# Kernel optimization log

Measured on AMD Instinct MI355X. Metric: run time of the kernel, lower is better.

Reference implementation:

```python
import jax, jax.numpy as jnp
import numpy as np
from jax import lax

B, N, R, L = 16, 256, 24, 32
MEAN_STOP_TIME_S = 60.0
AVG_TRANSFER_WAIT_TIME_S = 300.0
SYMMETRIC_ROUTES = True
INF = jnp.inf


def setup_inputs() -> dict:
    key = jax.random.key(0)
    k1, k2, k3 = jax.random.split(key, 3)
    drive_times = jax.random.uniform(k1, (B, N, N), jnp.float32) * 1000.0 + 30.0
    demand = jax.random.uniform(k2, (B, N, N), jnp.float32) * 10.0
    demand = demand * (1.0 - jnp.eye(N, dtype=jnp.float32))  # no self-demand
    batch_routes = jax.random.randint(k3, (B, R, L), 0, N, dtype=jnp.int32)
    return {"drive_times": drive_times, "demand": demand, "batch_routes": batch_routes}


def _route_edges_and_legs(routes, dtm):
    # routes: [B,R,L] node ids (no -1 padding in this setup); dtm: [B,N,N]
    b = jnp.arange(B)[:, None, None]
    sf, st = routes[:, :, :-1], routes[:, :, 1:]
    leg_fwd = dtm[b, sf, st] + MEAN_STOP_TIME_S            # [B,R,L-1]
    zero = jnp.zeros((B, R, 1), dtm.dtype)
    cum_f = jnp.concatenate([zero, jnp.cumsum(leg_fwd, -1)], -1)  # [B,R,L]
    tri = jnp.triu(jnp.ones((L, L), dtype=bool), 1)
    # ride time from stop position i to position j>i along the route
    t_f = jnp.where(tri, cum_f[:, :, None, :] - cum_f[:, :, :, None], INF)
    b4 = jnp.arange(B)[:, None, None, None]
    src = jnp.broadcast_to(routes[:, :, :, None], (B, R, L, L))
    dst = jnp.broadcast_to(routes[:, :, None, :], (B, R, L, L))
    edge = jnp.full((B, N, N), INF, dtm.dtype)
    edge = edge.at[b4, src, dst].min(t_f)
    leg_rev = None
    if SYMMETRIC_ROUTES:
        leg_rev = dtm[b, st, sf] + MEAN_STOP_TIME_S        # reverse-direction legs
        cum_r = jnp.concatenate([zero, jnp.cumsum(leg_rev, -1)], -1)
        t_r = jnp.where(tri, cum_r[:, :, None, :] - cum_r[:, :, :, None], INF)
        edge = edge.at[b4, dst, src].min(t_r)              # ride from s_j back to s_i
    return edge, leg_fwd, leg_rev


def _floyd_warshall(edge):
    # batched FW, also tracking hop count of shortest paths
    idx = jnp.arange(N)
    dist = edge.at[:, idx, idx].set(0.0)
    offdiag = ~jnp.eye(N, dtype=bool)
    hops = jnp.where(jnp.isfinite(dist) & offdiag, 1.0, 0.0)

    def body(carry, k):
        d, h = carry
        dc = lax.dynamic_slice_in_dim(d, k, 1, axis=2)  # [B,N,1]
        dr = lax.dynamic_slice_in_dim(d, k, 1, axis=1)  # [B,1,N]
        hc = lax.dynamic_slice_in_dim(h, k, 1, axis=2)
        hr = lax.dynamic_slice_in_dim(h, k, 1, axis=1)
        alt = dc + dr
        better = alt < d
        return (jnp.where(better, alt, d), jnp.where(better, hc + hr, h)), None

    (dist, hops), _ = lax.scan(body, (dist, hops), idx)
    return dist, hops


def reference(drive_times, demand, batch_routes):
    edge, leg_fwd, leg_rev = _route_edges_and_legs(batch_routes, drive_times)
    dist, hops = _floyd_warshall(edge)
    nopath = jnp.isinf(dist)
    path_lens = jnp.where(nopath, 0.0, hops + 1.0)  # n nodes on path (diag -> 1)
    transfers = jnp.where(path_lens == 0.0, 0.0, path_lens - 2.0)
    trip_times = jnp.where(nopath, 0.0, dist + transfers * AVG_TRANSFER_WAIT_TIME_S)
    total_demand_time = (demand * trip_times).sum((1, 2))
    total_transfers = (demand * transfers).sum((1, 2))
    unserved_demand = jnp.where(nopath, demand, 0.0).sum((1, 2))
    total_demand = demand.sum((1, 2))
    n_disconnected = (nopath & (demand > 0)).sum((1, 2))
    buckets = [jnp.where(transfers == float(ii), demand, 0.0).sum((1, 2)) for ii in range(3)]
    d_un = jnp.where(transfers > 2.0, demand, 0.0).sum((1, 2)) + unserved_demand
    trips_at_transfers = jnp.stack(buckets + [d_un], axis=1)  # [B,4]
    total_route_time = leg_fwd.sum((1, 2))
    if SYMMETRIC_ROUTES:
        total_route_time = total_route_time + leg_rev.sum((1, 2))
    return (total_demand_time, total_route_time, trips_at_transfers,
            total_demand, unserved_demand, total_transfers, trip_times,
            n_disconnected)
```

## Files before the change

kernel.cpp:

```cpp
#include <hip/hip_runtime.h>

#define BB 16
#define NL 256
#define RR 24
#define LL 32
#define NN (NL*NL)
#define BNN (BB*NN)
#define TT 64

#define O_TDT 0
#define O_RT  16
#define O_TAT 32
#define O_TD  96
#define O_UNS 112
#define O_TTR 128
#define O_TT  144
#define O_ND  1048720

#define HSC 9.3132257461547852e-10
#define H2  1073741824.0
#define HMASK 8191

#define RIDX(r, c2) (((r)<<6) + ((((c2) ^ ((r)&31)))<<1))
#define LDD(A, r, c2) (*(double2*)&A[RIDX((r),(c2))])

__global__ __launch_bounds__(1024) void k_init(double2* __restrict__ dist2, float* __restrict__ acc){
    int idx = blockIdx.x*1024 + threadIdx.x;
    double inf = __builtin_huge_val();
    double2 v = make_double2(inf, inf);
    int q = (idx*2) & (NN-1);
    int r = q % 257;
    if (r == 0)   v.x = 0.0;
    if (r == 256) v.y = 0.0;
    dist2[idx] = v;
    if (blockIdx.x == 0 && threadIdx.x < 256) acc[threadIdx.x] = 0.f;
}

__global__ void k_routes(const float* __restrict__ dtm, const int* __restrict__ routes,
                         unsigned long long* __restrict__ dist, float* __restrict__ acc){
    int br = blockIdx.x; int b = br / RR, r = br % RR;
    int lane = threadIdx.x;
    __shared__ int   s[LL];
    __shared__ float lf[LL], lr[LL], cf[LL], cr[LL];
    if (lane < LL) s[lane] = routes[(b*RR + r)*LL + lane];
    __syncthreads();
    if (lane < LL-1){
        int a0 = s[lane], a1 = s[lane+1];
        const float* dt = dtm + b*NN;
        lf[lane] = dt[a0*NL + a1] + 60.0f;
        lr[lane] = dt[a1*NL + a0] + 60.0f;
    }
    __syncthreads();
    if (lane == 0){
        float af = 0.f, ar = 0.f;
        cf[0] = 0.f; cr[0] = 0.f;
        for (int l = 0; l < LL-1; l++){
            af += lf[l]; ar += lr[l];
            cf[l+1] = af; cr[l+1] = ar;
        }
        atomicAdd(&acc[b*16 + 1], af + ar);
    }
    __syncthreads();
    for (int p = lane; p < LL*LL; p += 64){
        int i = p >> 5, j = p & 31;
        if (j > i){
            double vf = (double)(cf[j] - cf[i]) + HSC;
            double vr = (double)(cr[j] - cr[i]) + HSC;
            atomicMin(&dist[b*NN + s[i]*NL + s[j]], (unsigned long long)__double_as_longlong(vf));
            atomicMin(&dist[b*NN + s[j]*NL + s[i]], (unsigned long long)__double_as_longlong(vr));
        }
    }
}

__global__ __launch_bounds__(512) void k_fw_round(
        const double* __restrict__ src, double* __restrict__ dst, int kb){
    int b  = blockIdx.y;
    int m  = blockIdx.x;
    int ti = m >> 2, tj = m & 3;
    int t  = threadIdx.x;
    int rp  = (t >> 4) * 2;
    int cch = t & 15;
    int c04 = cch * 4;
    __shared__ double KD[4096];
    __shared__ double BD[4096];
    const double* Kg = src + b*NN + kb*TT*(NL+1);
    const double* Bg = src + b*NN + kb*TT*NL + tj*TT;
    const double* Cg = src + b*NN + ti*TT*NL + kb*TT;
    const double* Dg = src + b*NN + ti*TT*NL + tj*TT;

    double c0[2][4], d0[2][4];
    #pragma unroll
    for (int i = 0; i < 2; i++){
        double2 ca = *(const double2*)(Cg + (rp+i)*NL + c04);
        double2 cb = *(const double2*)(Cg + (rp+i)*NL + c04 + 2);
        c0[i][0]=ca.x; c0[i][1]=ca.y; c0[i][2]=cb.x; c0[i][3]=cb.y;
        double2 da = *(const double2*)(Dg + (rp+i)*NL + c04);
        double2 db = *(const double2*)(Dg + (rp+i)*NL + c04 + 2);
        d0[i][0]=da.x; d0[i][1]=da.y; d0[i][2]=db.x; d0[i][3]=db.y;
    }

    #pragma unroll
    for (int u = 0; u < 2; u++){
        int fid = u*512 + t;
        int row = fid >> 4, cc = fid & 15;
        const double* kp = Kg + row*NL + cc*4;
        double2 k0 = *(const double2*)kp, k1 = *(const double2*)(kp+2);
        const double* bp = Bg + row*NL + cc*4;
        double2 b0 = *(const double2*)bp, b1 = *(const double2*)(bp+2);
        LDD(KD,row,cc*2)   = k0; LDD(KD,row,cc*2+1) = k1;
        LDD(BD,row,cc*2)   = b0; LDD(BD,row,cc*2+1) = b1;
    }
    __syncthreads();

    for (int skb = 0; skb < 4; skb++){
        int s0 = skb*16, sc2 = skb*8;
        if (t < 64){
            int i = t >> 2, jg = t & 3, rr = s0 + i, cb = sc2 + jg*2;
            double2 m0 = LDD(KD, rr, cb), m1 = LDD(KD, rr, cb+1);
            double md[4] = {m0.x, m0.y, m1.x, m1.y};
            #pragma unroll
            for (int k = 0; k < 16; k++){
                double rd[4];
                #pragma unroll
                for (int c = 0; c < 4; c++) rd[c] = __shfl(md[c], (k<<2)|jg);
                double cd = __shfl(md[k&3], (i<<2)|(k>>2));
                #pragma unroll
                for (int c = 0; c < 4; c++) md[c] = fmin(md[c], cd + rd[c]);
            }
            LDD(KD, rr, cb)   = make_double2(md[0], md[1]);
            LDD(KD, rr, cb+1) = make_double2(md[2], md[3]);
        }
        __syncthreads();
        double sd[4];
        int wrow, wc2;
        if (t < 256){
            int rsr = s0 + (t >> 4);
            wrow = rsr; wc2 = (t & 15)*2;
            double2 v0 = LDD(KD, rsr, wc2), v1 = LDD(KD, rsr, wc2+1);
            sd[0]=v0.x; sd[1]=v0.y; sd[2]=v1.x; sd[3]=v1.y;
            #pragma unroll
            for (int k = 0; k < 16; k++){
                double ad = KD[RIDX(rsr, sc2+(k>>1)) + (k&1)];
                double2 b0 = LDD(KD, s0+k, wc2), b1 = LDD(KD, s0+k, wc2+1);
                sd[0] = fmin(sd[0], ad + b0.x);
                sd[1] = fmin(sd[1], ad + b0.y);
                sd[2] = fmin(sd[2], ad + b1.x);
                sd[3] = fmin(sd[3], ad + b1.y);
            }
        } else {
            int t2 = t - 256;
            int csr = t2 >> 2;
            wrow = csr; wc2 = sc2 + (t2 & 3)*2;
            double2 v0 = LDD(KD, csr, wc2), v1 = LDD(KD, csr, wc2+1);
            sd[0]=v0.x; sd[1]=v0.y; sd[2]=v1.x; sd[3]=v1.y;
            #pragma unroll
            for (int k = 0; k < 16; k++){
                double ad = KD[RIDX(csr, sc2+(k>>1)) + (k&1)];
                double2 b0 = LDD(KD, s0+k, wc2), b1 = LDD(KD, s0+k, wc2+1);
                sd[0] = fmin(sd[0], ad + b0.x);
                sd[1] = fmin(sd[1], ad + b0.y);
                sd[2] = fmin(sd[2], ad + b1.x);
                sd[3] = fmin(sd[3], ad + b1.y);
            }
        }
        __syncthreads();
        LDD(KD, wrow, wc2)   = make_double2(sd[0], sd[1]);
        LDD(KD, wrow, wc2+1) = make_double2(sd[2], sd[3]);
        __syncthreads();
        double dd[2][4];
        #pragma unroll
        for (int i = 0; i < 2; i++){
            double2 v0 = LDD(KD, rp+i, cch*2), v1 = LDD(KD, rp+i, cch*2+1);
            dd[i][0]=v0.x; dd[i][1]=v0.y; dd[i][2]=v1.x; dd[i][3]=v1.y;
        }
        #pragma unroll
        for (int q4 = 0; q4 < 4; q4++){
            double a[2][4], bm[4][4];
            #pragma unroll
            for (int i = 0; i < 2; i++){
                double2 a0 = LDD(KD, rp+i, sc2+q4*2), a1 = LDD(KD, rp+i, sc2+q4*2+1);
                a[i][0]=a0.x; a[i][1]=a0.y; a[i][2]=a1.x; a[i][3]=a1.y;
            }
            int kr = s0 + q4*4;
            #pragma unroll
            for (int q = 0; q < 4; q++){
                double2 b0 = LDD(KD, kr+q, cch*2), b1 = LDD(KD, kr+q, cch*2+1);
                bm[q][0]=b0.x; bm[q][1]=b0.y; bm[q][2]=b1.x; bm[q][3]=b1.y;
            }
            #pragma unroll
            for (int q = 0; q < 4; q++)
            #pragma unroll
            for (int i = 0; i < 2; i++)
            #pragma unroll
            for (int j = 0; j < 4; j++)
                dd[i][j] = fmin(dd[i][j], a[i][q] + bm[q][j]);
        }
        __syncthreads();
        #pragma unroll
        for (int i = 0; i < 2; i++){
            LDD(KD, rp+i, cch*2)   = make_double2(dd[i][0], dd[i][1]);
            LDD(KD, rp+i, cch*2+1) = make_double2(dd[i][2], dd[i][3]);
        }
        __syncthreads();
    }

    double inf = __builtin_huge_val();
    double md[2][4];
    #pragma unroll
    for (int i = 0; i < 2; i++)
    #pragma unroll
    for (int j = 0; j < 4; j++) md[i][j] = inf;
    #pragma unroll 4
    for (int q4 = 0; q4 < 16; q4++){
        double a[2][4], bm[4][4];
        #pragma unroll
        for (int i = 0; i < 2; i++){
            double2 a0 = LDD(KD, rp+i, q4*2), a1 = LDD(KD, rp+i, q4*2+1);
            a[i][0]=a0.x; a[i][1]=a0.y; a[i][2]=a1.x; a[i][3]=a1.y;
        }
        int kr = q4*4;
        #pragma unroll
        for (int q = 0; q < 4; q++){
            double2 b0 = LDD(BD, kr+q, cch*2), b1 = LDD(BD, kr+q, cch*2+1);
            bm[q][0]=b0.x; bm[q][1]=b0.y; bm[q][2]=b1.x; bm[q][3]=b1.y;
        }
        #pragma unroll
        for (int q = 0; q < 4; q++)
        #pragma unroll
        for (int i = 0; i < 2; i++)
        #pragma unroll
        for (int j = 0; j < 4; j++)
            md[i][j] = fmin(md[i][j], a[i][q] + bm[q][j]);
    }
    __syncthreads();
    #pragma unroll
    for (int i = 0; i < 2; i++){
        LDD(BD, rp+i, cch*2)   = make_double2(md[i][0], md[i][1]);
        LDD(BD, rp+i, cch*2+1) = make_double2(md[i][2], md[i][3]);
        LDD(KD, rp+i, cch*2)   = make_double2(c0[i][0], c0[i][1]);
        LDD(KD, rp+i, cch*2+1) = make_double2(c0[i][2], c0[i][3]);
    }
    __syncthreads();

    double dd[2][4];
    #pragma unroll
    for (int i = 0; i < 2; i++)
    #pragma unroll
    for (int j = 0; j < 4; j++) dd[i][j] = d0[i][j];
    #pragma unroll 4
    for (int q4 = 0; q4 < 16; q4++){
        double a[2][4], bm[4][4];
        #pragma unroll
        for (int i = 0; i < 2; i++){
            double2 a0 = LDD(KD, rp+i, q4*2), a1 = LDD(KD, rp+i, q4*2+1);
            a[i][0]=a0.x; a[i][1]=a0.y; a[i][2]=a1.x; a[i][3]=a1.y;
        }
        int kr = q4*4;
        #pragma unroll
        for (int q = 0; q < 4; q++){
            double2 b0 = LDD(BD, kr+q, cch*2), b1 = LDD(BD, kr+q, cch*2+1);
            bm[q][0]=b0.x; bm[q][1]=b0.y; bm[q][2]=b1.x; bm[q][3]=b1.y;
        }
        #pragma unroll
        for (int q = 0; q < 4; q++)
        #pragma unroll
        for (int i = 0; i < 2; i++)
        #pragma unroll
        for (int j = 0; j < 4; j++)
            dd[i][j] = fmin(dd[i][j], a[i][q] + bm[q][j]);
    }
    double* Od = dst + b*NN + ti*TT*NL + tj*TT;
    #pragma unroll
    for (int i = 0; i < 2; i++){
        *(double2*)(Od + (rp+i)*NL + c04)     = make_double2(dd[i][0], dd[i][1]);
        *(double2*)(Od + (rp+i)*NL + c04 + 2) = make_double2(dd[i][2], dd[i][3]);
    }
}

__global__ __launch_bounds__(1024) void k_epi(const double2* __restrict__ dist2,
        const float4* __restrict__ demand4, float* __restrict__ out, float* __restrict__ acc){
    int b = blockIdx.y;
    int fid = (b*NN >> 2) + blockIdx.x*1024 + threadIdx.x;
    long long q2 = (long long)fid * 2;
    double2 va = dist2[q2], vb = dist2[q2+1];
    double vs[4] = {va.x, va.y, vb.x, vb.y};
    float4 mv = demand4[fid];
    float ms[4] = {mv.x, mv.y, mv.z, mv.w};
    float s0=0,s1=0,s2=0,s3=0,s4=0,s5=0,s6=0,s7=0,s8=0;
    float tts[4];
    #pragma unroll
    for (int e = 0; e < 4; e++){
        double v = vs[e];
        bool np = !(v < 1e37);
        double vv = np ? 0.0 : v;
        int h = (int)(((long long)(vv * H2)) & (long long)HMASK);
        float d = (float)vv;
        float dm = ms[e];
        float pl = np ? 0.f : (float)(h + 1);
        float tr = (pl == 0.f) ? 0.f : pl - 2.f;
        float tt = np ? 0.f : d + tr*300.f;
        tts[e] = tt;
        s0 += dm*tt;
        s1 += dm*tr;
        s2 += np ? dm : 0.f;
        s3 += dm;
        s4 += (np && dm > 0.f) ? 1.f : 0.f;
        s5 += (tr == 0.f) ? dm : 0.f;
        s6 += (tr == 1.f) ? dm : 0.f;
        s7 += (tr == 2.f) ? dm : 0.f;
        s8 += (tr > 2.f) ? dm : 0.f;
    }
    ((float4*)(out + O_TT))[fid] = make_float4(tts[0],tts[1],tts[2],tts[3]);
    #define RED(x) { x += __shfl_down(x,32); x += __shfl_down(x,16); x += __shfl_down(x,8); \
                     x += __shfl_down(x,4);  x += __shfl_down(x,2);  x += __shfl_down(x,1); }
    RED(s0) RED(s1) RED(s2) RED(s3) RED(s4) RED(s5) RED(s6) RED(s7) RED(s8)
    __shared__ float red[16][9];
    int w = threadIdx.x >> 6;
    if ((threadIdx.x & 63) == 0){
        red[w][0]=s0; red[w][1]=s1; red[w][2]=s2; red[w][3]=s3; red[w][4]=s4;
        red[w][5]=s5; red[w][6]=s6; red[w][7]=s7; red[w][8]=s8;
    }
    __syncthreads();
    if (threadIdx.x < 9){
        float v = 0.f;
        #pragma unroll
        for (int ww = 0; ww < 16; ww++) v += red[ww][threadIdx.x];
        int slot = (threadIdx.x == 0) ? 0 : threadIdx.x + 1;
        atomicAdd(&acc[b*16 + slot], v);
    }
    __syncthreads();
    __shared__ int isLast;
    if (threadIdx.x == 0){
        unsigned prev = atomicAdd((unsigned int*)(acc + 255), 1u);
        isLast = (prev == 255u) ? 1 : 0;
    }
    __syncthreads();
    if (isLast && threadIdx.x < BB){
        int bb = threadIdx.x;
        float a[10];
        #pragma unroll
        for (int s = 0; s < 10; s++) a[s] = atomicAdd(&acc[bb*16 + s], 0.f);
        out[O_TDT + bb] = a[0];
        out[O_RT  + bb] = a[1];
        out[O_TAT + 4*bb + 0] = a[6];
        out[O_TAT + 4*bb + 1] = a[7];
        out[O_TAT + 4*bb + 2] = a[8];
        out[O_TAT + 4*bb + 3] = a[9] + a[3];
        out[O_TD  + bb] = a[4];
        out[O_UNS + bb] = a[3];
        out[O_TTR + bb] = a[2];
        out[O_ND  + bb] = a[5];
    }
}

extern "C" void kernel_launch(void* const* d_in, const int* in_sizes, int n_in,
                              void* d_out, int out_size, void* d_ws, size_t ws_size,
                              hipStream_t stream){
    (void)in_sizes; (void)n_in; (void)out_size; (void)ws_size;
    const float* dtm    = (const float*)d_in[0];
    const float* demand = (const float*)d_in[1];
    const int*   routes = (const int*)d_in[2];
    float* out   = (float*)d_out;
    double* distA = (double*)d_ws;
    double* distB = distA + BNN;
    float*  acc   = (float*)(distB + BNN);

    k_init  <<<512, 1024, 0, stream>>>((double2*)distA, acc);
    k_routes<<<BB*RR,  64, 0, stream>>>(dtm, routes, (unsigned long long*)distA, acc);
    k_fw_round<<<dim3(16,BB), 512, 0, stream>>>(distA, distB, 0);
    k_fw_round<<<dim3(16,BB), 512, 0, stream>>>(distB, distA, 1);
    k_fw_round<<<dim3(16,BB), 512, 0, stream>>>(distA, distB, 2);
    k_fw_round<<<dim3(16,BB), 512, 0, stream>>>(distB, distA, 3);
    k_epi<<<dim3(16,BB), 1024, 0, stream>>>((const double2*)distA,
                                            (const float4*)demand, out, acc);
}
```

Baseline: 238.4 us.

## Double FW-round block size to 1024 threads with 2x2 per-thread tiles

```diff
diff --git a/kernel.cpp b/kernel.cpp
--- a/kernel.cpp
+++ b/kernel.cpp
@@ -23,6 +23,7 @@
 
 #define RIDX(r, c2) (((r)<<6) + ((((c2) ^ ((r)&31)))<<1))
 #define LDD(A, r, c2) (*(double2*)&A[RIDX((r),(c2))])
+#define ELEM(A, r, c) A[RIDX((r), (c)>>1) + ((c)&1)]
 
 __global__ __launch_bounds__(1024) void k_init(double2* __restrict__ dist2, float* __restrict__ acc){
     int idx = blockIdx.x*1024 + threadIdx.x;
@@ -72,15 +73,14 @@
     }
 }
 
-__global__ __launch_bounds__(512) void k_fw_round(
+__global__ __launch_bounds__(1024, 4) void k_fw_round(
         const double* __restrict__ src, double* __restrict__ dst, int kb){
     int b  = blockIdx.y;
     int m  = blockIdx.x;
     int ti = m >> 2, tj = m & 3;
     int t  = threadIdx.x;
-    int rp  = (t >> 4) * 2;
-    int cch = t & 15;
-    int c04 = cch * 4;
+    int r0 = (t >> 5) << 1;
+    int c2 = t & 31;
     __shared__ double KD[4096];
     __shared__ double BD[4096];
     const double* Kg = src + b*NN + kb*TT*(NL+1);
@@ -88,27 +88,19 @@
     const double* Cg = src + b*NN + ti*TT*NL + kb*TT;
     const double* Dg = src + b*NN + ti*TT*NL + tj*TT;
 
-    double c0[2][4], d0[2][4];
+    double2 c0[2], d0[2];
     #pragma unroll
     for (int i = 0; i < 2; i++){
-        double2 ca = *(const double2*)(Cg + (rp+i)*NL + c04);
-        double2 cb = *(const double2*)(Cg + (rp+i)*NL + c04 + 2);
-        c0[i][0]=ca.x; c0[i][1]=ca.y; c0[i][2]=cb.x; c0[i][3]=cb.y;
-        double2 da = *(const double2*)(Dg + (rp+i)*NL + c04);
-        double2 db = *(const double2*)(Dg + (rp+i)*NL + c04 + 2);
-        d0[i][0]=da.x; d0[i][1]=da.y; d0[i][2]=db.x; d0[i][3]=db.y;
+        c0[i] = *(const double2*)(Cg + (r0+i)*NL + c2*2);
+        d0[i] = *(const double2*)(Dg + (r0+i)*NL + c2*2);
     }
 
     #pragma unroll
     for (int u = 0; u < 2; u++){
-        int fid = u*512 + t;
-        int row = fid >> 4, cc = fid & 15;
-        const double* kp = Kg + row*NL + cc*4;
-        double2 k0 = *(const double2*)kp, k1 = *(const double2*)(kp+2);
-        const double* bp = Bg + row*NL + cc*4;
-        double2 b0 = *(const double2*)bp, b1 = *(const double2*)(bp+2);
-        LDD(KD,row,cc*2)   = k0; LDD(KD,row,cc*2+1) = k1;
-        LDD(BD,row,cc*2)   = b0; LDD(BD,row,cc*2+1) = b1;
+        int fid = u*1024 + t;
+        int row = fid >> 5, cc = fid & 31;
+        LDD(KD, row, cc) = *(const double2*)(Kg + row*NL + cc*2);
+        LDD(BD, row, cc) = *(const double2*)(Bg + row*NL + cc*2);
     }
     __syncthreads();
 
@@ -117,164 +109,118 @@
         if (t < 64){
             int i = t >> 2, jg = t & 3, rr = s0 + i, cb = sc2 + jg*2;
             double2 m0 = LDD(KD, rr, cb), m1 = LDD(KD, rr, cb+1);
-            double md[4] = {m0.x, m0.y, m1.x, m1.y};
+            double md4[4] = {m0.x, m0.y, m1.x, m1.y};
             #pragma unroll
             for (int k = 0; k < 16; k++){
                 double rd[4];
                 #pragma unroll
-                for (int c = 0; c < 4; c++) rd[c] = __shfl(md[c], (k<<2)|jg);
-                double cd = __shfl(md[k&3], (i<<2)|(k>>2));
+                for (int c = 0; c < 4; c++) rd[c] = __shfl(md4[c], (k<<2)|jg);
+                double cd = __shfl(md4[k&3], (i<<2)|(k>>2));
                 #pragma unroll
-                for (int c = 0; c < 4; c++) md[c] = fmin(md[c], cd + rd[c]);
+                for (int c = 0; c < 4; c++) md4[c] = fmin(md4[c], cd + rd[c]);
             }
-            LDD(KD, rr, cb)   = make_double2(md[0], md[1]);
-            LDD(KD, rr, cb+1) = make_double2(md[2], md[3]);
-        }
-        __syncthreads();
-        double sd[4];
-        int wrow, wc2;
-        if (t < 256){
-            int rsr = s0 + (t >> 4);
-            wrow = rsr; wc2 = (t & 15)*2;
-            double2 v0 = LDD(KD, rsr, wc2), v1 = LDD(KD, rsr, wc2+1);
-            sd[0]=v0.x; sd[1]=v0.y; sd[2]=v1.x; sd[3]=v1.y;
-            #pragma unroll
-            for (int k = 0; k < 16; k++){
-                double ad = KD[RIDX(rsr, sc2+(k>>1)) + (k&1)];
-                double2 b0 = LDD(KD, s0+k, wc2), b1 = LDD(KD, s0+k, wc2+1);
-                sd[0] = fmin(sd[0], ad + b0.x);
-                sd[1] = fmin(sd[1], ad + b0.y);
-                sd[2] = fmin(sd[2], ad + b1.x);
-                sd[3] = fmin(sd[3], ad + b1.y);
-            }
-        } else {
-            int t2 = t - 256;
-            int csr = t2 >> 2;
-            wrow = csr; wc2 = sc2 + (t2 & 3)*2;
-            double2 v0 = LDD(KD, csr, wc2), v1 = LDD(KD, csr, wc2+1);
-            sd[0]=v0.x; sd[1]=v0.y; sd[2]=v1.x; sd[3]=v1.y;
-            #pragma unroll
-            for (int k = 0; k < 16; k++){
-                double ad = KD[RIDX(csr, sc2+(k>>1)) + (k&1)];
-                double2 b0 = LDD(KD, s0+k, wc2), b1 = LDD(KD, s0+k, wc2+1);
-                sd[0] = fmin(sd[0], ad + b0.x);
-                sd[1] = fmin(sd[1], ad + b0.y);
-                sd[2] = fmin(sd[2], ad + b1.x);
-                sd[3] = fmin(sd[3], ad + b1.y);
-            }
-        }
-        __syncthreads();
-        LDD(KD, wrow, wc2)   = make_double2(sd[0], sd[1]);
-        LDD(KD, wrow, wc2+1) = make_double2(sd[2], sd[3]);
-        __syncthreads();
-        double dd[2][4];
-        #pragma unroll
-        for (int i = 0; i < 2; i++){
-            double2 v0 = LDD(KD, rp+i, cch*2), v1 = LDD(KD, rp+i, cch*2+1);
-            dd[i][0]=v0.x; dd[i][1]=v0.y; dd[i][2]=v1.x; dd[i][3]=v1.y;
-        }
+            LDD(KD, rr, cb)   = make_double2(md4[0], md4[1]);
+            LDD(KD, rr, cb+1) = make_double2(md4[2], md4[3]);
+        }
+        __syncthreads();
+        int rr_r = s0 + (t >> 6);
+        int cc_r = t & 63;
+        int rr_c = t >> 4;
+        int cc_c = s0 + (t & 15);
+        double sr = ELEM(KD, rr_r, cc_r);
+        double sc = ELEM(KD, rr_c, cc_c);
+        #pragma unroll
+        for (int k = 0; k < 16; k++){
+            double ar = ELEM(KD, rr_r, s0 + k);
+            double br = ELEM(KD, s0 + k, cc_r);
+            sr = fmin(sr, ar + br);
+            double acl = ELEM(KD, rr_c, s0 + k);
+            double bcl = ELEM(KD, s0 + k, cc_c);
+            sc = fmin(sc, acl + bcl);
+        }
+        __syncthreads();
+        ELEM(KD, rr_r, cc_r) = sr;
+        ELEM(KD, rr_c, cc_c) = sc;
+        __syncthreads();
+        double2 dd0 = LDD(KD, r0, c2), dd1 = LDD(KD, r0+1, c2);
+        double dd[2][2] = {{dd0.x, dd0.y}, {dd1.x, dd1.y}};
         #pragma unroll
         for (int q4 = 0; q4 < 4; q4++){
-            double a[2][4], bm[4][4];
+            int kr = s0 + q4*4;
+            double a[2][4]; double2 bm[4];
             #pragma unroll
             for (int i = 0; i < 2; i++){
-                double2 a0 = LDD(KD, rp+i, sc2+q4*2), a1 = LDD(KD, rp+i, sc2+q4*2+1);
+                double2 a0 = LDD(KD, r0+i, sc2+q4*2), a1 = LDD(KD, r0+i, sc2+q4*2+1);
                 a[i][0]=a0.x; a[i][1]=a0.y; a[i][2]=a1.x; a[i][3]=a1.y;
             }
-            int kr = s0 + q4*4;
-            #pragma unroll
-            for (int q = 0; q < 4; q++){
-                double2 b0 = LDD(KD, kr+q, cch*2), b1 = LDD(KD, kr+q, cch*2+1);
-                bm[q][0]=b0.x; bm[q][1]=b0.y; bm[q][2]=b1.x; bm[q][3]=b1.y;
+            #pragma unroll
+            for (int q = 0; q < 4; q++) bm[q] = LDD(KD, kr+q, c2);
+            #pragma unroll
+            for (int q = 0; q < 4; q++)
+            #pragma unroll
+            for (int i = 0; i < 2; i++){
+                dd[i][0] = fmin(dd[i][0], a[i][q] + bm[q].x);
+                dd[i][1] = fmin(dd[i][1], a[i][q] + bm[q].y);
             }
-            #pragma unroll
-            for (int q = 0; q < 4; q++)
-            #pragma unroll
-            for (int i = 0; i < 2; i++)
-            #pragma unroll
-            for (int j = 0; j < 4; j++)
-                dd[i][j] = fmin(dd[i][j], a[i][q] + bm[q][j]);
-        }
-        __syncthreads();
+        }
+        __syncthreads();
+        LDD(KD, r0,   c2) = make_double2(dd[0][0], dd[0][1]);
+        LDD(KD, r0+1, c2) = make_double2(dd[1][0], dd[1][1]);
+        __syncthreads();
+    }
+
+    double inf = __builtin_huge_val();
+    double md[2][2] = {{inf, inf}, {inf, inf}};
+    #pragma unroll 4
+    for (int q4 = 0; q4 < 16; q4++){
+        double a[2][4]; double2 bm[4];
         #pragma unroll
         for (int i = 0; i < 2; i++){
-            LDD(KD, rp+i, cch*2)   = make_double2(dd[i][0], dd[i][1]);
-            LDD(KD, rp+i, cch*2+1) = make_double2(dd[i][2], dd[i][3]);
-        }
-        __syncthreads();
-    }
-
-    double inf = __builtin_huge_val();
-    double md[2][4];
+            double2 a0 = LDD(KD, r0+i, q4*2), a1 = LDD(KD, r0+i, q4*2+1);
+            a[i][0]=a0.x; a[i][1]=a0.y; a[i][2]=a1.x; a[i][3]=a1.y;
+        }
+        int kr = q4*4;
+        #pragma unroll
+        for (int q = 0; q < 4; q++) bm[q] = LDD(BD, kr+q, c2);
+        #pragma unroll
+        for (int q = 0; q < 4; q++)
+        #pragma unroll
+        for (int i = 0; i < 2; i++){
+            md[i][0] = fmin(md[i][0], a[i][q] + bm[q].x);
+            md[i][1] = fmin(md[i][1], a[i][q] + bm[q].y);
+        }
+    }
+    __syncthreads();
+    LDD(BD, r0,   c2) = make_double2(md[0][0], md[0][1]);
+    LDD(BD, r0+1, c2) = make_double2(md[1][0], md[1][1]);
+    LDD(KD, r0,   c2) = c0[0];
+    LDD(KD, r0+1, c2) = c0[1];
+    __syncthreads();
+
+    double dd[2][2] = {{d0[0].x, d0[0].y}, {d0[1].x, d0[1].y}};
+    #pragma unroll 4
+    for (int q4 = 0; q4 < 16; q4++){
+        double a[2][4]; double2 bm[4];
+        #pragma unroll
+        for (int i = 0; i < 2; i++){
+            double2 a0 = LDD(KD, r0+i, q4*2), a1 = LDD(KD, r0+i, q4*2+1);
+            a[i][0]=a0.x; a[i][1]=a0.y; a[i][2]=a1.x; a[i][3]=a1.y;
+        }
+        int kr = q4*4;
+        #pragma unroll
+        for (int q = 0; q < 4; q++) bm[q] = LDD(BD, kr+q, c2);
+        #pragma unroll
+        for (int q = 0; q < 4; q++)
+        #pragma unroll
+        for (int i = 0; i < 2; i++){
+            dd[i][0] = fmin(dd[i][0], a[i][q] + bm[q].x);
+            dd[i][1] = fmin(dd[i][1], a[i][q] + bm[q].y);
+        }
+    }
+    double* Od = dst + b*NN + ti*TT*NL + tj*TT;
     #pragma unroll
     for (int i = 0; i < 2; i++)
-    #pragma unroll
-    for (int j = 0; j < 4; j++) md[i][j] = inf;
-    #pragma unroll 4
-    for (int q4 = 0; q4 < 16; q4++){
-        double a[2][4], bm[4][4];
-        #pragma unroll
-        for (int i = 0; i < 2; i++){
-            double2 a0 = LDD(KD, rp+i, q4*2), a1 = LDD(KD, rp+i, q4*2+1);
-            a[i][0]=a0.x; a[i][1]=a0.y; a[i][2]=a1.x; a[i][3]=a1.y;
-        }
-        int kr = q4*4;
-        #pragma unroll
-        for (int q = 0; q < 4; q++){
-            double2 b0 = LDD(BD, kr+q, cch*2), b1 = LDD(BD, kr+q, cch*2+1);
-            bm[q][0]=b0.x; bm[q][1]=b0.y; bm[q][2]=b1.x; bm[q][3]=b1.y;
-        }
-        #pragma unroll
-        for (int q = 0; q < 4; q++)
-        #pragma unroll
-        for (int i = 0; i < 2; i++)
-        #pragma unroll
-        for (int j = 0; j < 4; j++)
-            md[i][j] = fmin(md[i][j], a[i][q] + bm[q][j]);
-    }
-    __syncthreads();
-    #pragma unroll
-    for (int i = 0; i < 2; i++){
-        LDD(BD, rp+i, cch*2)   = make_double2(md[i][0], md[i][1]);
-        LDD(BD, rp+i, cch*2+1) = make_double2(md[i][2], md[i][3]);
-        LDD(KD, rp+i, cch*2)   = make_double2(c0[i][0], c0[i][1]);
-        LDD(KD, rp+i, cch*2+1) = make_double2(c0[i][2], c0[i][3]);
-    }
-    __syncthreads();
-
-    double dd[2][4];
-    #pragma unroll
-    for (int i = 0; i < 2; i++)
-    #pragma unroll
-    for (int j = 0; j < 4; j++) dd[i][j] = d0[i][j];
-    #pragma unroll 4
-    for (int q4 = 0; q4 < 16; q4++){
-        double a[2][4], bm[4][4];
-        #pragma unroll
-        for (int i = 0; i < 2; i++){
-            double2 a0 = LDD(KD, rp+i, q4*2), a1 = LDD(KD, rp+i, q4*2+1);
-            a[i][0]=a0.x; a[i][1]=a0.y; a[i][2]=a1.x; a[i][3]=a1.y;
-        }
-        int kr = q4*4;
-        #pragma unroll
-        for (int q = 0; q < 4; q++){
-            double2 b0 = LDD(BD, kr+q, cch*2), b1 = LDD(BD, kr+q, cch*2+1);
-            bm[q][0]=b0.x; bm[q][1]=b0.y; bm[q][2]=b1.x; bm[q][3]=b1.y;
-        }
-        #pragma unroll
-        for (int q = 0; q < 4; q++)
-        #pragma unroll
-        for (int i = 0; i < 2; i++)
-        #pragma unroll
-        for (int j = 0; j < 4; j++)
-            dd[i][j] = fmin(dd[i][j], a[i][q] + bm[q][j]);
-    }
-    double* Od = dst + b*NN + ti*TT*NL + tj*TT;
-    #pragma unroll
-    for (int i = 0; i < 2; i++){
-        *(double2*)(Od + (rp+i)*NL + c04)     = make_double2(dd[i][0], dd[i][1]);
-        *(double2*)(Od + (rp+i)*NL + c04 + 2) = make_double2(dd[i][2], dd[i][3]);
-    }
+        *(double2*)(Od + (r0+i)*NL + c2*2) = make_double2(dd[i][0], dd[i][1]);
 }
 
 __global__ __launch_bounds__(1024) void k_epi(const double2* __restrict__ dist2,
@@ -367,10 +313,10 @@
 
     k_init  <<<512, 1024, 0, stream>>>((double2*)distA, acc);
     k_routes<<<BB*RR,  64, 0, stream>>>(dtm, routes, (unsigned long long*)distA, acc);
-    k_fw_round<<<dim3(16,BB), 512, 0, stream>>>(distA, distB, 0);
-    k_fw_round<<<dim3(16,BB), 512, 0, stream>>>(distB, distA, 1);
-    k_fw_round<<<dim3(16,BB), 512, 0, stream>>>(distA, distB, 2);
-    k_fw_round<<<dim3(16,BB), 512, 0, stream>>>(distB, distA, 3);
+    k_fw_round<<<dim3(16,BB), 1024, 0, stream>>>(distA, distB, 0);
+    k_fw_round<<<dim3(16,BB), 1024, 0, stream>>>(distB, distA, 1);
+    k_fw_round<<<dim3(16,BB), 1024, 0, stream>>>(distA, distB, 2);
+    k_fw_round<<<dim3(16,BB), 1024, 0, stream>>>(distB, distA, 3);
     k_epi<<<dim3(16,BB), 1024, 0, stream>>>((const double2*)distA,
                                             (const float4*)demand, out, acc);
 }
```

Result: slower. 246.6 us (+3.4%).
